# Optimization experiments

Measured on AMD Instinct MI355X. Metric: run time of the kernel, lower is better.

Reference implementation:

```python
import jax, jax.numpy as jnp
import numpy as np

B, C, H, W = 16, 512, 96, 48
SE_C = C // 16  # se bottleneck = 32
BN_EPS = 1e-5


def setup_inputs() -> dict:
    key = jax.random.key(0)
    ks = jax.random.split(key, 16)
    s = 0.02
    return {
        "x": jax.random.normal(ks[0], (B, C, H, W), jnp.float32),
        # SE gate: C -> SE_C -> C (1x1 convs stored as dense matrices)
        "se_w1": jax.random.normal(ks[1], (SE_C, C), jnp.float32) * s,
        "se_b1": jnp.zeros((SE_C,), jnp.float32),
        "se_w2": jax.random.normal(ks[2], (C, SE_C), jnp.float32) * s,
        "se_b2": jnp.zeros((C,), jnp.float32),
        # g / theta / phi: 1x1 convs C -> 1 (weight is a C-vector, scalar bias)
        "g_w": jax.random.normal(ks[3], (C,), jnp.float32) * s,
        "g_b": jnp.zeros((), jnp.float32),
        "theta_w": jax.random.normal(ks[4], (C,), jnp.float32) * s,
        "theta_b": jnp.zeros((), jnp.float32),
        "phi_w": jax.random.normal(ks[5], (C,), jnp.float32) * s,
        "phi_b": jnp.zeros((), jnp.float32),
        # W: 1x1 conv 1 -> C, followed by BatchNorm2d(C) (inference stats).
        # NOTE: torch inits BN gamma/beta to 0 (output would be exactly x);
        # we use random gamma/beta so the whole graph contributes to output/grads.
        "W_w": jax.random.normal(ks[6], (C,), jnp.float32) * s,
        "W_b": jnp.zeros((C,), jnp.float32),
        "bn_gamma": jax.random.normal(ks[7], (C,), jnp.float32) * 0.1 + 1.0,
        "bn_beta": jax.random.normal(ks[8], (C,), jnp.float32) * 0.1,
        "bn_mean": jax.random.normal(ks[9], (C,), jnp.float32) * 0.1,
        "bn_var": jax.random.uniform(ks[10], (C,), jnp.float32, 0.5, 1.5),
    }


def reference(x, se_w1, se_b1, se_w2, se_b2, g_w, g_b, theta_w, theta_b,
              phi_w, phi_b, W_w, W_b, bn_gamma, bn_beta, bn_mean, bn_var):
    b, c, h, w = x.shape
    n = h * w
    # SE channel gate on global-avg-pooled features
    xp = x.mean(axis=(2, 3))                                  # (b, c)
    hid = jax.nn.relu(xp @ se_w1.T + se_b1)                   # (b, se_c)
    gate = jax.nn.sigmoid(hid @ se_w2.T + se_b2)              # (b, c)
    xc = gate[:, :, None, None] * x                           # (b, c, h, w)
    # 1x1 C->1 projections, flattened over spatial positions
    g_x = jnp.einsum('bchw,c->bhw', xc, g_w).reshape(b, n) + g_b       # (b, n)
    th = jnp.einsum('bchw,c->bhw', xc, theta_w).reshape(b, n) + theta_b
    ph = jnp.einsum('bchw,c->bhw', xc, phi_w).reshape(b, n) + phi_b
    # f = theta phi^T / N; y = f g. inter_channels==1 => rank-1, contract phi.g first
    s = jnp.sum(ph * g_x, axis=-1, keepdims=True) / n          # (b, 1)
    y = (th * s).reshape(b, 1, h, w)                           # (b, 1, h, w)
    # W: 1x1 conv 1->C then BatchNorm2d (inference form)
    wy = y * W_w[None, :, None, None] + W_b[None, :, None, None]
    inv = bn_gamma / jnp.sqrt(bn_var + BN_EPS)
    wy = (wy - bn_mean[None, :, None, None]) * inv[None, :, None, None] \
         + bn_beta[None, :, None, None]
    return wy + x
```

## Files before the change

kernel.cpp:

```cpp
#include <hip/hip_runtime.h>
#include <math.h>

#define BB   16
#define CCH  512
#define HWN  4608
#define HW4  1152
#define HW2  2304
#define NSE  32
#define BN_EPS 1e-5f

typedef float f32x4 __attribute__((ext_vector_type(4)));

__global__ __launch_bounds__(256) void k_mean(const float* __restrict__ x,
                                              float* __restrict__ xp) {
    int wave = threadIdx.x >> 6;
    int lane = threadIdx.x & 63;
    int row = blockIdx.x * 4 + wave;
    const float4* xr = (const float4*)x + (size_t)row * HW4;
    float s = 0.f;
    #pragma unroll
    for (int k = 0; k < 18; ++k) {
        float4 v = xr[lane + k * 64];
        s += v.x + v.y + v.z + v.w;
    }
    #pragma unroll
    for (int off = 32; off > 0; off >>= 1)
        s += __shfl_down(s, off);
    if (lane == 0) xp[row] = s * (1.0f / (float)HWN);
}

__global__ __launch_bounds__(512) void k_gate(
    const float* __restrict__ xp,
    const float* __restrict__ se_w1, const float* __restrict__ se_b1,
    const float* __restrict__ se_w2, const float* __restrict__ se_b2,
    const float* __restrict__ g_w, const float* __restrict__ theta_w,
    const float* __restrict__ phi_w,
    float* __restrict__ tw, float* __restrict__ pw, float* __restrict__ gw) {
    __shared__ float xs[CCH];
    __shared__ float hs[NSE];
    int b = blockIdx.x, t = threadIdx.x;
    int wave = t >> 6, lane = t & 63;
    xs[t] = xp[b * CCH + t];
    __syncthreads();
    #pragma unroll
    for (int i = 0; i < 4; ++i) {
        int h = wave * 4 + i;
        const float* wr = se_w1 + h * CCH;
        float a = 0.f;
        #pragma unroll
        for (int k = 0; k < 8; ++k)
            a += wr[lane + 64 * k] * xs[lane + 64 * k];
        #pragma unroll
        for (int off = 32; off > 0; off >>= 1)
            a += __shfl_down(a, off);
        if (lane == 0) {
            a += se_b1[h];
            hs[h] = a > 0.f ? a : 0.f;
        }
    }
    __syncthreads();
    float a = se_b2[t];
    const float* wr = se_w2 + t * NSE;
    #pragma unroll
    for (int j = 0; j < NSE; ++j) a += wr[j] * hs[j];
    float gate = 1.f / (1.f + expf(-a));
    int idx = b * CCH + t;
    tw[idx] = gate * theta_w[t];
    pw[idx] = gate * phi_w[t];
    gw[idx] = gate * g_w[t];
}

__global__ __launch_bounds__(128) void k_proj(
    const float* __restrict__ x,
    const float* __restrict__ tw, const float* __restrict__ pw,
    const float* __restrict__ gw,
    float* __restrict__ th_part, float* __restrict__ ph_part,
    float* __restrict__ gx_part) {
    __shared__ float tws[128], pws[128], gws[128];
    int t = threadIdx.x;
    int b = blockIdx.z;
    int c0 = blockIdx.y * 128;
    int p2 = blockIdx.x * 128 + t;
    int wi = b * CCH + c0 + t;
    tws[t] = tw[wi]; pws[t] = pw[wi]; gws[t] = gw[wi];
    __syncthreads();
    const float2* xr = (const float2*)x + (size_t)(b * CCH + c0) * HW2 + p2;
    float2 tha = {0.f, 0.f}, pha = {0.f, 0.f}, gxa = {0.f, 0.f};
    #pragma unroll 8
    for (int c = 0; c < 128; ++c) {
        float2 v = xr[(size_t)c * HW2];
        float tc = tws[c], pc = pws[c], gc = gws[c];
        tha.x += tc * v.x; tha.y += tc * v.y;
        pha.x += pc * v.x; pha.y += pc * v.y;
        gxa.x += gc * v.x; gxa.y += gc * v.y;
    }
    size_t oi = (size_t)(blockIdx.y * BB + b) * HW2 + p2;
    ((float2*)th_part)[oi] = tha;
    ((float2*)ph_part)[oi] = pha;
    ((float2*)gx_part)[oi] = gxa;
}

__global__ __launch_bounds__(256) void k_scale(
    const float* __restrict__ th_part, const float* __restrict__ ph_part,
    const float* __restrict__ gx_part,
    const float* __restrict__ theta_b, const float* __restrict__ phi_b,
    const float* __restrict__ g_b,
    float* __restrict__ ths) {
    __shared__ float red[256];
    int b = blockIdx.x, t = threadIdx.x;
    float pb = phi_b[0], gb = g_b[0];
    const float4* php = (const float4*)ph_part;
    const float4* gxp = (const float4*)gx_part;
    float acc = 0.f;
    for (int i = t; i < HW4; i += 256) {
        float4 ph = {pb, pb, pb, pb};
        float4 gx = {gb, gb, gb, gb};
        #pragma unroll
        for (int k = 0; k < 4; ++k) {
            size_t oi = (size_t)(k * BB + b) * HW4 + i;
            float4 pv = php[oi];
            float4 gv = gxp[oi];
            ph.x += pv.x; ph.y += pv.y; ph.z += pv.z; ph.w += pv.w;
            gx.x += gv.x; gx.y += gv.y; gx.z += gv.z; gx.w += gv.w;
        }
        acc += ph.x * gx.x + ph.y * gx.y + ph.z * gx.z + ph.w * gx.w;
    }
    red[t] = acc;
    __syncthreads();
    for (int off = 128; off > 0; off >>= 1) {
        if (t < off) red[t] += red[t + off];
        __syncthreads();
    }
    float s = red[0] * (1.0f / (float)HWN);
    float tb = theta_b[0];
    const float4* thp = (const float4*)th_part;
    float4* out4 = (float4*)ths;
    for (int i = t; i < HW4; i += 256) {
        float4 th = {tb, tb, tb, tb};
        #pragma unroll
        for (int k = 0; k < 4; ++k) {
            float4 tv = thp[(size_t)(k * BB + b) * HW4 + i];
            th.x += tv.x; th.y += tv.y; th.z += tv.z; th.w += tv.w;
        }
        float4 o;
        o.x = th.x * s; o.y = th.y * s; o.z = th.z * s; o.w = th.w * s;
        out4[(size_t)b * HW4 + i] = o;
    }
}

__global__ __launch_bounds__(256) void k_out(
    const float* __restrict__ x, const float* __restrict__ ths,
    const float* __restrict__ W_w, const float* __restrict__ W_b,
    const float* __restrict__ bn_gamma, const float* __restrict__ bn_beta,
    const float* __restrict__ bn_mean, const float* __restrict__ bn_var,
    float* __restrict__ out) {
    int wave = threadIdx.x >> 6;
    int lane = threadIdx.x & 63;
    int c = blockIdx.x * 4 + wave;
    int b = blockIdx.y;
    float inv = bn_gamma[c] * rsqrtf(bn_var[c] + BN_EPS);
    float A = W_w[c] * inv;
    float Dc = (W_b[c] - bn_mean[c]) * inv + bn_beta[c];
    const float4* xr = (const float4*)x + (size_t)(b * CCH + c) * HW4;
    const float4* tr = (const float4*)ths + (size_t)b * HW4;
    f32x4* orow = (f32x4*)out + (size_t)(b * CCH + c) * HW4;
    #pragma unroll
    for (int k = 0; k < 18; ++k) {
        int i = lane + k * 64;
        float4 xv = xr[i];
        float4 tv = tr[i];
        f32x4 o;
        o.x = xv.x + tv.x * A + Dc;
        o.y = xv.y + tv.y * A + Dc;
        o.z = xv.z + tv.z * A + Dc;
        o.w = xv.w + tv.w * A + Dc;
        __builtin_nontemporal_store(o, &orow[i]);
    }
}

extern "C" void kernel_launch(void* const* d_in, const int* in_sizes, int n_in,
                              void* d_out, int out_size, void* d_ws, size_t ws_size,
                              hipStream_t stream) {
    const float* x       = (const float*)d_in[0];
    const float* se_w1   = (const float*)d_in[1];
    const float* se_b1   = (const float*)d_in[2];
    const float* se_w2   = (const float*)d_in[3];
    const float* se_b2   = (const float*)d_in[4];
    const float* g_w     = (const float*)d_in[5];
    const float* g_b     = (const float*)d_in[6];
    const float* theta_w = (const float*)d_in[7];
    const float* theta_b = (const float*)d_in[8];
    const float* phi_w   = (const float*)d_in[9];
    const float* phi_b   = (const float*)d_in[10];
    const float* W_w     = (const float*)d_in[11];
    const float* W_b     = (const float*)d_in[12];
    const float* bn_g    = (const float*)d_in[13];
    const float* bn_b    = (const float*)d_in[14];
    const float* bn_m    = (const float*)d_in[15];
    const float* bn_v    = (const float*)d_in[16];
    float* out = (float*)d_out;

    float* ws      = (float*)d_ws;
    float* xp      = ws;
    float* tw      = ws + 8192;
    float* pw      = ws + 16384;
    float* gw      = ws + 24576;
    float* th_part = ws + 32768;
    float* ph_part = ws + 32768 + 294912;
    float* gx_part = ws + 32768 + 2 * 294912;
    float* ths     = ws + 32768 + 3 * 294912;

    k_mean<<<BB * CCH / 4, 256, 0, stream>>>(x, xp);
    k_gate<<<BB, CCH, 0, stream>>>(xp, se_w1, se_b1, se_w2, se_b2,
                                   g_w, theta_w, phi_w, tw, pw, gw);
    dim3 gc(18, 4, BB);
    k_proj<<<gc, 128, 0, stream>>>(x, tw, pw, gw, th_part, ph_part, gx_part);
    k_scale<<<BB, 256, 0, stream>>>(th_part, ph_part, gx_part,
                                    theta_b, phi_b, g_b, ths);
    dim3 gd(CCH / 4, BB);
    k_out<<<gd, 256, 0, stream>>>(x, ths, W_w, W_b, bn_g, bn_b, bn_m, bn_v, out);
}
```

Baseline: 339.1 us.

## Fuse all five stages into one cooperative persistent kernel with grid syncs

Replaces the five separate launches (mean, gate, projection, scale, output) with one cooperative kernel of 576 blocks that runs each stage in turn, separated by grid-wide syncs and thread fences. This removes per-launch overhead and the gaps between kernels. In exchange, stages that use only 16 blocks (gate, scale) leave most of the grid waiting at a barrier, and every grid.sync adds its own latency. The kernel falls back to the old multi-kernel path if cooperative launch or occupancy is insufficient.

```diff
diff --git a/kernel.cpp b/kernel.cpp
--- a/kernel.cpp
+++ b/kernel.cpp
@@ -1,5 +1,8 @@
 #include <hip/hip_runtime.h>
+#include <hip/hip_cooperative_groups.h>
 #include <math.h>
+
+namespace cg = cooperative_groups;
 
 #define BB   16
 #define CCH  512
@@ -9,7 +12,180 @@
 #define NSE  32
 #define BN_EPS 1e-5f
 
+#define NBLK 576
+#define NTHR 256
+
 typedef float f32x4 __attribute__((ext_vector_type(4)));
+
+__global__ __launch_bounds__(NTHR, 4) void k_fused(
+    const float* __restrict__ x,
+    const float* __restrict__ se_w1, const float* __restrict__ se_b1,
+    const float* __restrict__ se_w2, const float* __restrict__ se_b2,
+    const float* __restrict__ g_w,   const float* __restrict__ g_b,
+    const float* __restrict__ theta_w, const float* __restrict__ theta_b,
+    const float* __restrict__ phi_w, const float* __restrict__ phi_b,
+    const float* __restrict__ W_w,   const float* __restrict__ W_b,
+    const float* __restrict__ bn_g,  const float* __restrict__ bn_b,
+    const float* __restrict__ bn_m,  const float* __restrict__ bn_v,
+    float* __restrict__ out,
+    float* __restrict__ xp, float* __restrict__ tw, float* __restrict__ pw,
+    float* __restrict__ gwv, float* __restrict__ th_part,
+    float* __restrict__ ph_part, float* __restrict__ gx_part,
+    float* __restrict__ ths)
+{
+    cg::grid_group grid = cg::this_grid();
+    int blk = blockIdx.x, t = threadIdx.x;
+    int wave = t >> 6, lane = t & 63;
+    int gwid = blk * 4 + wave;
+
+    for (int r = gwid; r < BB * CCH; r += NBLK * 4) {
+        const float4* xr = (const float4*)x + (size_t)r * HW4;
+        float s = 0.f;
+        #pragma unroll 6
+        for (int k = 0; k < 18; ++k) {
+            float4 v = xr[lane + k * 64];
+            s += v.x + v.y + v.z + v.w;
+        }
+        #pragma unroll
+        for (int off = 32; off > 0; off >>= 1)
+            s += __shfl_down(s, off);
+        if (lane == 0) xp[r] = s * (1.0f / (float)HWN);
+    }
+    __threadfence();
+    grid.sync();
+
+    if (blk < BB) {
+        __shared__ float xs[CCH];
+        __shared__ float hs[NSE];
+        xs[t]       = xp[blk * CCH + t];
+        xs[t + 256] = xp[blk * CCH + 256 + t];
+        __syncthreads();
+        #pragma unroll
+        for (int i = 0; i < 8; ++i) {
+            int h = wave * 8 + i;
+            const float* wr = se_w1 + h * CCH;
+            float a = 0.f;
+            #pragma unroll
+            for (int k = 0; k < 8; ++k)
+                a += wr[lane + 64 * k] * xs[lane + 64 * k];
+            #pragma unroll
+            for (int off = 32; off > 0; off >>= 1)
+                a += __shfl_down(a, off);
+            if (lane == 0) {
+                a += se_b1[h];
+                hs[h] = a > 0.f ? a : 0.f;
+            }
+        }
+        __syncthreads();
+        for (int c = t; c < CCH; c += NTHR) {
+            float a = se_b2[c];
+            const float* wr = se_w2 + c * NSE;
+            #pragma unroll
+            for (int j = 0; j < NSE; ++j) a += wr[j] * hs[j];
+            float gate = 1.f / (1.f + expf(-a));
+            int idx = blk * CCH + c;
+            tw[idx]  = gate * theta_w[c];
+            pw[idx]  = gate * phi_w[c];
+            gwv[idx] = gate * g_w[c];
+        }
+    }
+    __threadfence();
+    grid.sync();
+
+    {
+        int b = blk / 36, rem = blk % 36, ch = rem / 9, pb = rem % 9;
+        int c0 = ch * 128;
+        int p2 = pb * 256 + t;
+        __shared__ float tws[128], pws[128], gws[128];
+        if (t < 128) {
+            int wi = b * CCH + c0 + t;
+            tws[t] = tw[wi]; pws[t] = pw[wi]; gws[t] = gwv[wi];
+        }
+        __syncthreads();
+        const float2* xr = (const float2*)x + (size_t)(b * CCH + c0) * HW2 + p2;
+        float2 tha = {0.f, 0.f}, pha = {0.f, 0.f}, gxa = {0.f, 0.f};
+        #pragma unroll 4
+        for (int c = 0; c < 128; ++c) {
+            float2 v = xr[(size_t)c * HW2];
+            float tc = tws[c], pc = pws[c], gc = gws[c];
+            tha.x += tc * v.x; tha.y += tc * v.y;
+            pha.x += pc * v.x; pha.y += pc * v.y;
+            gxa.x += gc * v.x; gxa.y += gc * v.y;
+        }
+        size_t oi = (size_t)(ch * BB + b) * HW2 + p2;
+        ((float2*)th_part)[oi] = tha;
+        ((float2*)ph_part)[oi] = pha;
+        ((float2*)gx_part)[oi] = gxa;
+    }
+    __threadfence();
+    grid.sync();
+
+    if (blk < BB) {
+        __shared__ float red[NTHR];
+        int b = blk;
+        float pb_ = phi_b[0], gb_ = g_b[0];
+        const float4* php = (const float4*)ph_part;
+        const float4* gxp = (const float4*)gx_part;
+        float acc = 0.f;
+        for (int i = t; i < HW4; i += NTHR) {
+            float4 ph = {pb_, pb_, pb_, pb_};
+            float4 gx = {gb_, gb_, gb_, gb_};
+            #pragma unroll
+            for (int k = 0; k < 4; ++k) {
+                size_t oi = (size_t)(k * BB + b) * HW4 + i;
+                float4 pv = php[oi];
+                float4 gv = gxp[oi];
+                ph.x += pv.x; ph.y += pv.y; ph.z += pv.z; ph.w += pv.w;
+                gx.x += gv.x; gx.y += gv.y; gx.z += gv.z; gx.w += gv.w;
+            }
+            acc += ph.x * gx.x + ph.y * gx.y + ph.z * gx.z + ph.w * gx.w;
+        }
+        red[t] = acc;
+        __syncthreads();
+        for (int off = 128; off > 0; off >>= 1) {
+            if (t < off) red[t] += red[t + off];
+            __syncthreads();
+        }
+        float s = red[0] * (1.0f / (float)HWN);
+        float tb = theta_b[0];
+        const float4* thp = (const float4*)th_part;
+        float4* o4 = (float4*)ths;
+        for (int i = t; i < HW4; i += NTHR) {
+            float4 th = {tb, tb, tb, tb};
+            #pragma unroll
+            for (int k = 0; k < 4; ++k) {
+                float4 tv = thp[(size_t)(k * BB + b) * HW4 + i];
+                th.x += tv.x; th.y += tv.y; th.z += tv.z; th.w += tv.w;
+            }
+            float4 o = {th.x * s, th.y * s, th.z * s, th.w * s};
+            o4[(size_t)b * HW4 + i] = o;
+        }
+    }
+    __threadfence();
+    grid.sync();
+
+    for (int r = gwid; r < BB * CCH; r += NBLK * 4) {
+        int b = r >> 9, c = r & 511;
+        float inv = bn_g[c] * rsqrtf(bn_v[c] + BN_EPS);
+        float A = W_w[c] * inv;
+        float Dc = (W_b[c] - bn_m[c]) * inv + bn_b[c];
+        const float4* xr = (const float4*)x + (size_t)r * HW4;
+        const float4* tr = (const float4*)ths + (size_t)b * HW4;
+        f32x4* orow = (f32x4*)out + (size_t)r * HW4;
+        #pragma unroll 6
+        for (int k = 0; k < 18; ++k) {
+            int i = lane + k * 64;
+            float4 xv = xr[i];
+            float4 tv = tr[i];
+            f32x4 o;
+            o.x = xv.x + tv.x * A + Dc;
+            o.y = xv.y + tv.y * A + Dc;
+            o.z = xv.z + tv.z * A + Dc;
+            o.w = xv.w + tv.w * A + Dc;
+            __builtin_nontemporal_store(o, &orow[i]);
+        }
+    }
+}
 
 __global__ __launch_bounds__(256) void k_mean(const float* __restrict__ x,
                                               float* __restrict__ xp) {
@@ -204,17 +380,46 @@
     float* xp      = ws;
     float* tw      = ws + 8192;
     float* pw      = ws + 16384;
-    float* gw      = ws + 24576;
+    float* gwv     = ws + 24576;
     float* th_part = ws + 32768;
     float* ph_part = ws + 32768 + 294912;
     float* gx_part = ws + 32768 + 2 * 294912;
     float* ths     = ws + 32768 + 3 * 294912;
 
+    static int coop = -1;
+    if (coop < 0) {
+        int nb = 0;
+        hipError_t e = hipOccupancyMaxActiveBlocksPerMultiprocessor(
+            &nb, (const void*)k_fused, NTHR, 0);
+        int dev = 0;
+        hipGetDevice(&dev);
+        hipDeviceProp_t prop;
+        hipError_t e2 = hipGetDeviceProperties(&prop, dev);
+        coop = (e == hipSuccess && e2 == hipSuccess && prop.cooperativeLaunch &&
+                nb * prop.multiProcessorCount >= NBLK) ? 1 : 0;
+    }
+
+    if (coop == 1) {
+        void* args[] = {
+            (void*)&x,
+            (void*)&se_w1, (void*)&se_b1, (void*)&se_w2, (void*)&se_b2,
+            (void*)&g_w, (void*)&g_b, (void*)&theta_w, (void*)&theta_b,
+            (void*)&phi_w, (void*)&phi_b, (void*)&W_w, (void*)&W_b,
+            (void*)&bn_g, (void*)&bn_b, (void*)&bn_m, (void*)&bn_v,
+            (void*)&out,
+            (void*)&xp, (void*)&tw, (void*)&pw, (void*)&gwv,
+            (void*)&th_part, (void*)&ph_part, (void*)&gx_part, (void*)&ths
+        };
+        hipLaunchCooperativeKernel((const void*)k_fused, dim3(NBLK), dim3(NTHR),
+                                   args, 0, stream);
+        return;
+    }
+
     k_mean<<<BB * CCH / 4, 256, 0, stream>>>(x, xp);
     k_gate<<<BB, CCH, 0, stream>>>(xp, se_w1, se_b1, se_w2, se_b2,
-                                   g_w, theta_w, phi_w, tw, pw, gw);
+                                   g_w, theta_w, phi_w, tw, pw, gwv);
     dim3 gc(18, 4, BB);
-    k_proj<<<gc, 128, 0, stream>>>(x, tw, pw, gw, th_part, ph_part, gx_part);
+    k_proj<<<gc, 128, 0, stream>>>(x, tw, pw, gwv, th_part, ph_part, gx_part);
     k_scale<<<BB, 256, 0, stream>>>(th_part, ph_part, gx_part,
                                     theta_b, phi_b, g_b, ths);
     dim3 gd(CCH / 4, BB);
```

Measured after the change: 840.9 us. 148% more time.
